# Kernel optimization log

Hardware: AMD Instinct MI355X
Metric: run time of the kernel (lower is better)

Reference implementation:

```python
import jax, jax.numpy as jnp
import numpy as np

C = 256
CQK = C // 8  # reduction_ratio = 8


def setup_inputs() -> dict:
    key = jax.random.key(0)
    ks = jax.random.split(key, 8)
    B, H, W = 8, 64, 64
    x = jax.random.normal(ks[0], (B, C, H, W), dtype=jnp.float32)
    s_in = 1.0 / np.sqrt(C)
    Wq = jax.random.normal(ks[1], (CQK, C), dtype=jnp.float32) * s_in
    bq = jax.random.normal(ks[2], (CQK,), dtype=jnp.float32) * 0.01
    Wk = jax.random.normal(ks[3], (CQK, C), dtype=jnp.float32) * s_in
    bk = jax.random.normal(ks[4], (CQK,), dtype=jnp.float32) * 0.01
    Wv = jax.random.normal(ks[5], (C, C), dtype=jnp.float32) * s_in
    bv = jax.random.normal(ks[6], (C,), dtype=jnp.float32) * 0.01
    gamma = jax.random.normal(ks[7], (1,), dtype=jnp.float32) * 0.1
    return {"x": x, "Wq": Wq, "bq": bq, "Wk": Wk, "bk": bk,
            "Wv": Wv, "bv": bv, "gamma": gamma}


def reference(x, Wq, bq, Wk, bk, Wv, bv, gamma):
    B, Cc, H, W = x.shape
    N = H * W
    xf = x.reshape(B, Cc, N)  # [B, C, N]
    # 1x1 convs == per-pixel linear maps over channels
    q = jnp.einsum('qc,bcn->bnq', Wq, xf) + bq            # [B, N, Cqk]
    k = jnp.einsum('kc,bcn->bkn', Wk, xf) + bk[None, :, None]  # [B, Cqk, N]
    v = jnp.einsum('vc,bcn->bvn', Wv, xf) + bv[None, :, None]  # [B, C, N]
    # unscaled attention scores, softmax over keys (last dim)
    scores = jax.nn.softmax(jnp.einsum('bnq,bqm->bnm', q, k), axis=-1)  # [B, N, N]
    # out[b,c,n] = sum_m v[b,c,m] * scores[b,n,m]  (torch: value @ scores^T)
    attn = jnp.einsum('bvm,bnm->bvn', v, scores)          # [B, C, N]
    out = gamma[0] * attn.reshape(B, Cc, H, W) + x
    return out
```

## Files before the change

kernel.cpp:

```cpp
#include <hip/hip_runtime.h>

static constexpr int B_   = 8;
static constexpr int C_   = 256;
static constexpr int CQK_ = 32;
static constexpr int N_   = 4096;

typedef __attribute__((ext_vector_type(4))) float f32x4;
typedef __attribute__((ext_vector_type(8))) short short8;
typedef __attribute__((ext_vector_type(2))) unsigned int u32x2;
typedef unsigned short ushort_t;

__device__ inline unsigned short f2bf(float f) {
    unsigned u = __float_as_uint(f);
    return (unsigned short)((u + 0x7FFFu + ((u >> 16) & 1u)) >> 16);
}
__device__ inline unsigned packbf(float lo, float hi) {
    return (unsigned)f2bf(lo) | ((unsigned)f2bf(hi) << 16);
}

__device__ inline int swzbits(int m) {
    return ((m & 3) << 5) | (((m >> 3) & 1) << 4);
}

template <int OFF>
__device__ inline u32x2 tr8(unsigned a) {
    u32x2 d;
    asm volatile("ds_read_b64_tr_b16 %0, %1 offset:%2"
                 : "=v"(d) : "v"(a), "i"(OFF));
    return d;
}

__device__ inline short8 mk8(u32x2 lo, u32x2 hi) {
    union { unsigned u[4]; short8 s; } v;
    v.u[0] = lo.x; v.u[1] = lo.y; v.u[2] = hi.x; v.u[3] = hi.y;
    return v.s;
}

__global__ __launch_bounds__(256) void prep_kernel(
    const float* __restrict__ Wq, const float* __restrict__ bq,
    const float* __restrict__ Wk, const float* __restrict__ bk,
    const float* __restrict__ Wv, const float* __restrict__ bv,
    ushort_t* __restrict__ Wall, float* __restrict__ ball)
{
    const int r = blockIdx.x;
    const int t = threadIdx.x;
    const float* src;
    float bsrc;
    if (r < 32)      { src = Wq + (size_t)r * C_;        bsrc = bq[r]; }
    else if (r < 64) { src = Wk + (size_t)(r - 32) * C_; bsrc = bk[r - 32]; }
    else             { src = Wv + (size_t)(r - 64) * C_; bsrc = bv[r - 64]; }
    Wall[(size_t)r * C_ + t] = f2bf(src[t]);
    if (t == 0) ball[r] = bsrc;
}

__global__ __launch_bounds__(256) void proj_kernel(
    const float* __restrict__ x,
    const ushort_t* __restrict__ Wall, const float* __restrict__ ball,
    ushort_t* __restrict__ Qb, ushort_t* __restrict__ Kb, ushort_t* __restrict__ Vb)
{
    __shared__ __align__(16) unsigned char xs[C_ * 128];
    typedef __attribute__((address_space(3))) unsigned char lds_byte;
    const unsigned sbase = (unsigned)(size_t)(lds_byte*)xs;

    const int b  = blockIdx.x & 7;
    const int n0 = (blockIdx.x >> 3) << 6;
    const int t  = threadIdx.x;

    {
        const int cst = t >> 4;
        const int n4  = (t & 15) << 2;
        const float* xb = x + (size_t)b * C_ * N_ + n0;
        #pragma unroll
        for (int i = 0; i < 16; ++i) {
            const int c = 16 * i + cst;
            float4 v = *(const float4*)(xb + (size_t)c * N_ + n4);
            u32x2 pk;
            pk.x = packbf(v.x, v.y);
            pk.y = packbf(v.z, v.w);
            *(u32x2*)(xs + c * 128 + ((n4 * 2) ^ swzbits(c))) = pk;
        }
    }
    __syncthreads();

    const int l  = t & 63, w = t >> 6;
    const int li = l & 15, g = l >> 4;
    const int rr = li >> 2, ss = l & 3;
    const int swz_tr = (rr << 5) | ((g & 1) << 4);
    const int ocb = 80 * w;

    f32x4 acc[5][4];
    #pragma unroll
    for (int i = 0; i < 5; ++i)
        #pragma unroll
        for (int j = 0; j < 4; ++j) acc[i][j] = (f32x4){0.f, 0.f, 0.f, 0.f};

    #pragma unroll 2
    for (int kg = 0; kg < 8; ++kg) {
        u32x2 pb[4][2];
        #pragma unroll
        for (int jn = 0; jn < 4; ++jn) {
            unsigned a = sbase + (32 * kg + 8 * g + rr) * 128
                       + ((32 * jn + 8 * ss) ^ swz_tr);
            pb[jn][0] = tr8<0>(a);
            pb[jn][1] = tr8<512>(a);
        }
        short8 af[5];
        #pragma unroll
        for (int tm = 0; tm < 5; ++tm)
            af[tm] = *(const short8*)(Wall + (size_t)(ocb + 16 * tm + li) * C_
                                      + 32 * kg + 8 * g);
        asm volatile("s_waitcnt lgkmcnt(0)" ::: "memory");
        __builtin_amdgcn_sched_barrier(0);
        #pragma unroll
        for (int tm = 0; tm < 5; ++tm) {
            #pragma unroll
            for (int jn = 0; jn < 4; ++jn) {
                short8 Bf = mk8(pb[jn][0], pb[jn][1]);
                acc[tm][jn] = __builtin_amdgcn_mfma_f32_16x16x32_bf16(
                                  af[tm], Bf, acc[tm][jn], 0, 0, 0);
            }
        }
    }

    #pragma unroll
    for (int tm = 0; tm < 5; ++tm) {
        const int oc0 = ocb + 16 * tm + 4 * g;
        float4 bias = *(const float4*)(ball + oc0);
        #pragma unroll
        for (int jn = 0; jn < 4; ++jn) {
            const int n = n0 + 16 * jn + li;
            f32x4 a = acc[tm][jn];
            u32x2 pk;
            pk.x = packbf(a[0] + bias.x, a[1] + bias.y);
            pk.y = packbf(a[2] + bias.z, a[3] + bias.w);
            if (oc0 < 32) {
                *(u32x2*)(Qb + (size_t)(b * N_ + n) * CQK_ + oc0) = pk;
            } else if (oc0 < 64) {
                *(u32x2*)(Kb + (size_t)(b * N_ + n) * CQK_ + (oc0 - 32)) = pk;
            } else {
                char* dst = (char*)Vb + (size_t)(b * N_ + n) * 512
                          + (((oc0 - 64) * 2) ^ swzbits(n));
                *(u32x2*)dst = pk;
            }
        }
    }
}

__global__ __launch_bounds__(256) void attn_kernel(
    const float* __restrict__ x,
    const ushort_t* __restrict__ Qb, const ushort_t* __restrict__ Kb,
    const ushort_t* __restrict__ Vb,
    const float* __restrict__ gamma, float* __restrict__ out)
{
    __shared__ __align__(16) unsigned char smem[32768 + 8192 + 256];
    unsigned char* Pl = smem + 32768;
    float* rsl = (float*)(smem + 32768 + 8192);

    typedef __attribute__((address_space(3))) unsigned char lds_byte;
    const unsigned sbase = (unsigned)(size_t)(lds_byte*)smem;

    const int b  = blockIdx.x & 7;
    const int n0 = (blockIdx.x >> 3) << 6;
    const int t  = threadIdx.x;
    const int l  = t & 63, w = t >> 6;
    const int li = l & 15, g = l >> 4;
    const int rr = li >> 2, ss = l & 3;
    const int hq = w & 1,  hc = w >> 1;
    const int swz_tr = (rr << 5) | ((g & 1) << 4);

    short8 qf = *(const short8*)(Qb + (size_t)(b * N_ + n0 + 16 * w + li) * CQK_ + 8 * g);

    f32x4 acc[2][8];
    #pragma unroll
    for (int i = 0; i < 2; ++i)
        #pragma unroll
        for (int j = 0; j < 8; ++j) acc[i][j] = (f32x4){0.f, 0.f, 0.f, 0.f};
    float rs0 = 0.f, rs1 = 0.f, rs2 = 0.f, rs3 = 0.f;

    const ushort_t* Kbb = Kb + (size_t)(b * N_) * CQK_;
    const char* Vgb = (const char*)Vb + (size_t)(b * N_) * 512;
    const f32x4 zf = {0.f, 0.f, 0.f, 0.f};

    for (int m0 = 0; m0 < N_; m0 += 64) {
        short8 kf[4];
        #pragma unroll
        for (int jm = 0; jm < 4; ++jm)
            kf[jm] = *(const short8*)(Kbb + (size_t)(m0 + 16 * jm + li) * CQK_ + 8 * g);

        {
            const char* gsrc = Vgb + (size_t)m0 * 512 + w * 1024 + l * 16;
            #pragma unroll
            for (int i = 0; i < 8; ++i)
                __builtin_amdgcn_global_load_lds(
                    (const __attribute__((address_space(1))) unsigned int*)(gsrc + i * 4096),
                    (__attribute__((address_space(3))) unsigned int*)(smem + w * 1024 + i * 4096),
                    16, 0, 0);
        }

        #pragma unroll
        for (int jm = 0; jm < 4; ++jm) {
            f32x4 s = __builtin_amdgcn_mfma_f32_16x16x32_bf16(qf, kf[jm], zf, 0, 0, 0);
            float p0 = __expf(s[0]), p1 = __expf(s[1]);
            float p2 = __expf(s[2]), p3 = __expf(s[3]);
            rs0 += p0; rs1 += p1; rs2 += p2; rs3 += p3;
            const int m = 16 * jm + li;
            u32x2 pu; pu.x = packbf(p0, p1); pu.y = packbf(p2, p3);
            *(u32x2*)(Pl + m * 128 + ((32 * w + 8 * g) ^ swzbits(m))) = pu;
        }
        __syncthreads();

        #pragma unroll
        for (int kb = 0; kb < 2; ++kb) {
            u32x2 pa[2][2], vbf[8][2];
            #pragma unroll
            for (int jq = 0; jq < 2; ++jq) {
                unsigned a = sbase + 32768u
                           + (32 * kb + 8 * g + rr) * 128
                           + ((64 * hq + 32 * jq + 8 * ss) ^ swz_tr);
                pa[jq][0] = tr8<0>(a);
                pa[jq][1] = tr8<512>(a);
            }
            #pragma unroll
            for (int jc = 0; jc < 8; ++jc) {
                unsigned a = sbase
                           + (32 * kb + 8 * g + rr) * 512
                           + ((256 * hc + 32 * jc + 8 * ss) ^ swz_tr);
                vbf[jc][0] = tr8<0>(a);
                vbf[jc][1] = tr8<2048>(a);
            }
            asm volatile("s_waitcnt lgkmcnt(0)" ::: "memory");
            __builtin_amdgcn_sched_barrier(0);
            #pragma unroll
            for (int jq = 0; jq < 2; ++jq) {
                short8 A = mk8(pa[jq][0], pa[jq][1]);
                #pragma unroll
                for (int jc = 0; jc < 8; ++jc) {
                    short8 Bf = mk8(vbf[jc][0], vbf[jc][1]);
                    acc[jq][jc] = __builtin_amdgcn_mfma_f32_16x16x32_bf16(
                                      A, Bf, acc[jq][jc], 0, 0, 0);
                }
            }
        }
        __syncthreads();
    }

    float rsv[4] = {rs0, rs1, rs2, rs3};
    #pragma unroll
    for (int r = 0; r < 4; ++r) {
        float v = rsv[r];
        v += __shfl_xor(v, 1, 64);
        v += __shfl_xor(v, 2, 64);
        v += __shfl_xor(v, 4, 64);
        v += __shfl_xor(v, 8, 64);
        rsv[r] = v;
    }
    if (li == 0) {
        rsl[16 * w + 4 * g + 0] = rsv[0];
        rsl[16 * w + 4 * g + 1] = rsv[1];
        rsl[16 * w + 4 * g + 2] = rsv[2];
        rsl[16 * w + 4 * g + 3] = rsv[3];
    }
    __syncthreads();

    float inv[2][4];
    #pragma unroll
    for (int jq = 0; jq < 2; ++jq)
        #pragma unroll
        for (int r = 0; r < 4; ++r)
            inv[jq][r] = 1.0f / rsl[32 * hq + 16 * jq + 4 * g + r];

    const float gm = gamma[0];
    #pragma unroll
    for (int jq = 0; jq < 2; ++jq)
        #pragma unroll
        for (int jc = 0; jc < 8; ++jc) {
            const int c = 128 * hc + 16 * jc + li;
            const size_t rowoff = (size_t)(b * C_ + c) * N_
                                + n0 + 32 * hq + 16 * jq + 4 * g;
            float4 xv = *(const float4*)(x + rowoff);
            f32x4 a = acc[jq][jc];
            float4 o;
            o.x = gm * a[0] * inv[jq][0] + xv.x;
            o.y = gm * a[1] * inv[jq][1] + xv.y;
            o.z = gm * a[2] * inv[jq][2] + xv.z;
            o.w = gm * a[3] * inv[jq][3] + xv.w;
            *(float4*)(out + rowoff) = o;
        }
}

extern "C" void kernel_launch(void* const* d_in, const int* in_sizes, int n_in,
                              void* d_out, int out_size, void* d_ws, size_t ws_size,
                              hipStream_t stream)
{
    const float* x     = (const float*)d_in[0];
    const float* Wq    = (const float*)d_in[1];
    const float* bq    = (const float*)d_in[2];
    const float* Wk    = (const float*)d_in[3];
    const float* bk    = (const float*)d_in[4];
    const float* Wv    = (const float*)d_in[5];
    const float* bv    = (const float*)d_in[6];
    const float* gamma = (const float*)d_in[7];
    float* out = (float*)d_out;

    ushort_t* ws = (ushort_t*)d_ws;
    ushort_t* Qb   = ws;
    ushort_t* Kb   = Qb + (size_t)B_ * N_ * CQK_;
    ushort_t* Vb   = Kb + (size_t)B_ * N_ * CQK_;
    ushort_t* Wall = Vb + (size_t)B_ * N_ * C_;
    float*    ball = (float*)(Wall + (size_t)320 * C_);

    prep_kernel<<<320, 256, 0, stream>>>(Wq, bq, Wk, bk, Wv, bv, Wall, ball);
    proj_kernel<<<B_ * (N_ / 64), 256, 0, stream>>>(x, Wall, ball, Qb, Kb, Vb);
    attn_kernel<<<B_ * (N_ / 64), 256, 0, stream>>>(x, Qb, Kb, Vb, gamma, out);
}
```

Before: 151.1 us.

## Store V channel-major and load V fragments directly from global in attention

The projection kernel now writes V transposed as [B, C, N] bf16 and computes transposed MFMA tiles for V, so the attention kernel can read V B-fragments straight from global memory into registers instead of staging them through LDS with transposing reads. Each wave now keeps its own private P tile in padded LDS, covering both query halves, which removes the block-wide __syncthreads in the key loop. Row sums are reduced with shuffles and ds_bpermute rather than a shared-memory pass. The trade-off is that each wave computes the QK scores twice (redundant exp work across the hc halves) and issues more global V loads that rely on the cache, in exchange for less LDS traffic and fewer block-wide barriers.

```diff
diff --git a/kernel.cpp b/kernel.cpp
--- a/kernel.cpp
+++ b/kernel.cpp
@@ -56,7 +56,7 @@
 __global__ __launch_bounds__(256) void proj_kernel(
     const float* __restrict__ x,
     const ushort_t* __restrict__ Wall, const float* __restrict__ ball,
-    ushort_t* __restrict__ Qb, ushort_t* __restrict__ Kb, ushort_t* __restrict__ Vb)
+    ushort_t* __restrict__ Qb, ushort_t* __restrict__ Kb, ushort_t* __restrict__ Vt)
 {
     __shared__ __align__(16) unsigned char xs[C_ * 128];
     typedef __attribute__((address_space(3))) unsigned char lds_byte;
@@ -86,7 +86,6 @@
     const int li = l & 15, g = l >> 4;
     const int rr = li >> 2, ss = l & 3;
     const int swz_tr = (rr << 5) | ((g & 1) << 4);
-    const int ocb = 80 * w;
 
     f32x4 acc[5][4];
     #pragma unroll
@@ -107,41 +106,48 @@
         short8 af[5];
         #pragma unroll
         for (int tm = 0; tm < 5; ++tm)
-            af[tm] = *(const short8*)(Wall + (size_t)(ocb + 16 * tm + li) * C_
+            af[tm] = *(const short8*)(Wall + (size_t)(16 * (4 * tm + w) + li) * C_
                                       + 32 * kg + 8 * g);
         asm volatile("s_waitcnt lgkmcnt(0)" ::: "memory");
         __builtin_amdgcn_sched_barrier(0);
         #pragma unroll
-        for (int tm = 0; tm < 5; ++tm) {
-            #pragma unroll
-            for (int jn = 0; jn < 4; ++jn) {
-                short8 Bf = mk8(pb[jn][0], pb[jn][1]);
+        for (int jn = 0; jn < 4; ++jn) {
+            short8 Bf = mk8(pb[jn][0], pb[jn][1]);
+            acc[0][jn] = __builtin_amdgcn_mfma_f32_16x16x32_bf16(
+                             af[0], Bf, acc[0][jn], 0, 0, 0);
+            #pragma unroll
+            for (int tm = 1; tm < 5; ++tm)
                 acc[tm][jn] = __builtin_amdgcn_mfma_f32_16x16x32_bf16(
-                                  af[tm], Bf, acc[tm][jn], 0, 0, 0);
-            }
-        }
-    }
-
-    #pragma unroll
-    for (int tm = 0; tm < 5; ++tm) {
-        const int oc0 = ocb + 16 * tm + 4 * g;
+                                  Bf, af[tm], acc[tm][jn], 0, 0, 0);
+        }
+    }
+
+    {
+        const int oc0 = 16 * w + 4 * g;
         float4 bias = *(const float4*)(ball + oc0);
+        ushort_t* dst = (w < 2) ? Qb : Kb;
+        const int col = (w < 2) ? oc0 : (oc0 - 32);
         #pragma unroll
         for (int jn = 0; jn < 4; ++jn) {
             const int n = n0 + 16 * jn + li;
-            f32x4 a = acc[tm][jn];
+            f32x4 a = acc[0][jn];
             u32x2 pk;
             pk.x = packbf(a[0] + bias.x, a[1] + bias.y);
             pk.y = packbf(a[2] + bias.z, a[3] + bias.w);
-            if (oc0 < 32) {
-                *(u32x2*)(Qb + (size_t)(b * N_ + n) * CQK_ + oc0) = pk;
-            } else if (oc0 < 64) {
-                *(u32x2*)(Kb + (size_t)(b * N_ + n) * CQK_ + (oc0 - 32)) = pk;
-            } else {
-                char* dst = (char*)Vb + (size_t)(b * N_ + n) * 512
-                          + (((oc0 - 64) * 2) ^ swzbits(n));
-                *(u32x2*)dst = pk;
-            }
+            *(u32x2*)(dst + (size_t)(b * N_ + n) * CQK_ + col) = pk;
+        }
+    }
+    #pragma unroll
+    for (int tm = 1; tm < 5; ++tm) {
+        const int c  = 16 * (4 * tm + w) + li - 64;
+        const float bc = ball[64 + c];
+        #pragma unroll
+        for (int jn = 0; jn < 4; ++jn) {
+            f32x4 a = acc[tm][jn];
+            u32x2 pk;
+            pk.x = packbf(a[0] + bc, a[1] + bc);
+            pk.y = packbf(a[2] + bc, a[3] + bc);
+            *(u32x2*)(Vt + (size_t)(b * C_ + c) * N_ + n0 + 16 * jn + 4 * g) = pk;
         }
     }
 }
@@ -149,36 +155,34 @@
 __global__ __launch_bounds__(256) void attn_kernel(
     const float* __restrict__ x,
     const ushort_t* __restrict__ Qb, const ushort_t* __restrict__ Kb,
-    const ushort_t* __restrict__ Vb,
+    const ushort_t* __restrict__ Vt,
     const float* __restrict__ gamma, float* __restrict__ out)
 {
-    __shared__ __align__(16) unsigned char smem[32768 + 8192 + 256];
-    unsigned char* Pl = smem + 32768;
-    float* rsl = (float*)(smem + 32768 + 8192);
-
-    typedef __attribute__((address_space(3))) unsigned char lds_byte;
-    const unsigned sbase = (unsigned)(size_t)(lds_byte*)smem;
+    __shared__ __align__(16) unsigned char Pl[4 * 32 * 144];
 
     const int b  = blockIdx.x & 7;
     const int n0 = (blockIdx.x >> 3) << 6;
     const int t  = threadIdx.x;
     const int l  = t & 63, w = t >> 6;
     const int li = l & 15, g = l >> 4;
-    const int rr = li >> 2, ss = l & 3;
     const int hq = w & 1,  hc = w >> 1;
-    const int swz_tr = (rr << 5) | ((g & 1) << 4);
-
-    short8 qf = *(const short8*)(Qb + (size_t)(b * N_ + n0 + 16 * w + li) * CQK_ + 8 * g);
+    unsigned char* Pw = Pl + w * 4608;
+    const int xorq = (li & 1) << 4;
+
+    short8 qf[2];
+    #pragma unroll
+    for (int jq = 0; jq < 2; ++jq)
+        qf[jq] = *(const short8*)(Qb + (size_t)(b * N_ + n0 + 32 * hq + 16 * jq + li) * CQK_ + 8 * g);
 
     f32x4 acc[2][8];
     #pragma unroll
     for (int i = 0; i < 2; ++i)
         #pragma unroll
         for (int j = 0; j < 8; ++j) acc[i][j] = (f32x4){0.f, 0.f, 0.f, 0.f};
-    float rs0 = 0.f, rs1 = 0.f, rs2 = 0.f, rs3 = 0.f;
+    float rs[2] = {0.f, 0.f};
 
     const ushort_t* Kbb = Kb + (size_t)(b * N_) * CQK_;
-    const char* Vgb = (const char*)Vb + (size_t)(b * N_) * 512;
+    const ushort_t* Vtb = Vt + (size_t)b * C_ * N_;
     const f32x4 zf = {0.f, 0.f, 0.f, 0.f};
 
     for (int m0 = 0; m0 < N_; m0 += 64) {
@@ -186,88 +190,76 @@
         #pragma unroll
         for (int jm = 0; jm < 4; ++jm)
             kf[jm] = *(const short8*)(Kbb + (size_t)(m0 + 16 * jm + li) * CQK_ + 8 * g);
+        short8 v0[8];
+        #pragma unroll
+        for (int jc = 0; jc < 8; ++jc)
+            v0[jc] = *(const short8*)(Vtb + (size_t)(128 * hc + 16 * jc + li) * N_
+                                      + m0 + 8 * g);
+
+        #pragma unroll
+        for (int jm = 0; jm < 4; ++jm) {
+            #pragma unroll
+            for (int jq = 0; jq < 2; ++jq) {
+                f32x4 s = __builtin_amdgcn_mfma_f32_16x16x32_bf16(kf[jm], qf[jq], zf, 0, 0, 0);
+                float p0 = __expf(s[0]), p1 = __expf(s[1]);
+                float p2 = __expf(s[2]), p3 = __expf(s[3]);
+                rs[jq] += p0 + p1 + p2 + p3;
+                u32x2 pk; pk.x = packbf(p0, p1); pk.y = packbf(p2, p3);
+                *(u32x2*)(Pw + (16 * jq + li) * 144
+                             + ((32 * jm + 8 * g) ^ xorq)) = pk;
+            }
+        }
+        asm volatile("s_waitcnt lgkmcnt(0)" ::: "memory");
+        __builtin_amdgcn_sched_barrier(0);
+
+        short8 v1[8];
+        #pragma unroll
+        for (int jc = 0; jc < 8; ++jc)
+            v1[jc] = *(const short8*)(Vtb + (size_t)(128 * hc + 16 * jc + li) * N_
+                                      + m0 + 32 + 8 * g);
 
         {
-            const char* gsrc = Vgb + (size_t)m0 * 512 + w * 1024 + l * 16;
-            #pragma unroll
-            for (int i = 0; i < 8; ++i)
-                __builtin_amdgcn_global_load_lds(
-                    (const __attribute__((address_space(1))) unsigned int*)(gsrc + i * 4096),
-                    (__attribute__((address_space(3))) unsigned int*)(smem + w * 1024 + i * 4096),
-                    16, 0, 0);
-        }
-
-        #pragma unroll
-        for (int jm = 0; jm < 4; ++jm) {
-            f32x4 s = __builtin_amdgcn_mfma_f32_16x16x32_bf16(qf, kf[jm], zf, 0, 0, 0);
-            float p0 = __expf(s[0]), p1 = __expf(s[1]);
-            float p2 = __expf(s[2]), p3 = __expf(s[3]);
-            rs0 += p0; rs1 += p1; rs2 += p2; rs3 += p3;
-            const int m = 16 * jm + li;
-            u32x2 pu; pu.x = packbf(p0, p1); pu.y = packbf(p2, p3);
-            *(u32x2*)(Pl + m * 128 + ((32 * w + 8 * g) ^ swzbits(m))) = pu;
-        }
-        __syncthreads();
-
-        #pragma unroll
-        for (int kb = 0; kb < 2; ++kb) {
-            u32x2 pa[2][2], vbf[8][2];
-            #pragma unroll
-            for (int jq = 0; jq < 2; ++jq) {
-                unsigned a = sbase + 32768u
-                           + (32 * kb + 8 * g + rr) * 128
-                           + ((64 * hq + 32 * jq + 8 * ss) ^ swz_tr);
-                pa[jq][0] = tr8<0>(a);
-                pa[jq][1] = tr8<512>(a);
-            }
-            #pragma unroll
-            for (int jc = 0; jc < 8; ++jc) {
-                unsigned a = sbase
-                           + (32 * kb + 8 * g + rr) * 512
-                           + ((256 * hc + 32 * jc + 8 * ss) ^ swz_tr);
-                vbf[jc][0] = tr8<0>(a);
-                vbf[jc][1] = tr8<2048>(a);
-            }
-            asm volatile("s_waitcnt lgkmcnt(0)" ::: "memory");
-            __builtin_amdgcn_sched_barrier(0);
-            #pragma unroll
-            for (int jq = 0; jq < 2; ++jq) {
-                short8 A = mk8(pa[jq][0], pa[jq][1]);
+            short8 pa[2];
+            #pragma unroll
+            for (int jq = 0; jq < 2; ++jq)
+                pa[jq] = *(const short8*)(Pw + (16 * jq + li) * 144
+                                             + ((16 * g) ^ xorq));
+            #pragma unroll
+            for (int jq = 0; jq < 2; ++jq)
                 #pragma unroll
-                for (int jc = 0; jc < 8; ++jc) {
-                    short8 Bf = mk8(vbf[jc][0], vbf[jc][1]);
+                for (int jc = 0; jc < 8; ++jc)
                     acc[jq][jc] = __builtin_amdgcn_mfma_f32_16x16x32_bf16(
-                                      A, Bf, acc[jq][jc], 0, 0, 0);
-                }
-            }
-        }
-        __syncthreads();
-    }
-
-    float rsv[4] = {rs0, rs1, rs2, rs3};
-    #pragma unroll
-    for (int r = 0; r < 4; ++r) {
-        float v = rsv[r];
-        v += __shfl_xor(v, 1, 64);
-        v += __shfl_xor(v, 2, 64);
-        v += __shfl_xor(v, 4, 64);
-        v += __shfl_xor(v, 8, 64);
-        rsv[r] = v;
-    }
-    if (li == 0) {
-        rsl[16 * w + 4 * g + 0] = rsv[0];
-        rsl[16 * w + 4 * g + 1] = rsv[1];
-        rsl[16 * w + 4 * g + 2] = rsv[2];
-        rsl[16 * w + 4 * g + 3] = rsv[3];
-    }
-    __syncthreads();
-
+                                      pa[jq], v0[jc], acc[jq][jc], 0, 0, 0);
+        }
+        {
+            short8 pa[2];
+            #pragma unroll
+            for (int jq = 0; jq < 2; ++jq)
+                pa[jq] = *(const short8*)(Pw + (16 * jq + li) * 144
+                                             + ((64 + 16 * g) ^ xorq));
+            #pragma unroll
+            for (int jq = 0; jq < 2; ++jq)
+                #pragma unroll
+                for (int jc = 0; jc < 8; ++jc)
+                    acc[jq][jc] = __builtin_amdgcn_mfma_f32_16x16x32_bf16(
+                                      pa[jq], v1[jc], acc[jq][jc], 0, 0, 0);
+        }
+    }
+
+    #pragma unroll
+    for (int jq = 0; jq < 2; ++jq) {
+        rs[jq] += __shfl_xor(rs[jq], 16, 64);
+        rs[jq] += __shfl_xor(rs[jq], 32, 64);
+    }
     float inv[2][4];
     #pragma unroll
     for (int jq = 0; jq < 2; ++jq)
         #pragma unroll
-        for (int r = 0; r < 4; ++r)
-            inv[jq][r] = 1.0f / rsl[32 * hq + 16 * jq + 4 * g + r];
+        for (int r = 0; r < 4; ++r) {
+            int v = __builtin_amdgcn_ds_bpermute((4 * g + r) * 4,
+                                                 __float_as_int(rs[jq]));
+            inv[jq][r] = 1.0f / __int_as_float(v);
+        }
 
     const float gm = gamma[0];
     #pragma unroll
@@ -305,11 +297,11 @@
     ushort_t* ws = (ushort_t*)d_ws;
     ushort_t* Qb   = ws;
     ushort_t* Kb   = Qb + (size_t)B_ * N_ * CQK_;
-    ushort_t* Vb   = Kb + (size_t)B_ * N_ * CQK_;
-    ushort_t* Wall = Vb + (size_t)B_ * N_ * C_;
+    ushort_t* Vt   = Kb + (size_t)B_ * N_ * CQK_;
+    ushort_t* Wall = Vt + (size_t)B_ * C_ * N_;
     float*    ball = (float*)(Wall + (size_t)320 * C_);
 
     prep_kernel<<<320, 256, 0, stream>>>(Wq, bq, Wk, bk, Wv, bv, Wall, ball);
-    proj_kernel<<<B_ * (N_ / 64), 256, 0, stream>>>(x, Wall, ball, Qb, Kb, Vb);
-    attn_kernel<<<B_ * (N_ / 64), 256, 0, stream>>>(x, Qb, Kb, Vb, gamma, out);
-}
+    proj_kernel<<<B_ * (N_ / 64), 256, 0, stream>>>(x, Wall, ball, Qb, Kb, Vt);
+    attn_kernel<<<B_ * (N_ / 64), 256, 0, stream>>>(x, Qb, Kb, Vt, gamma, out);
+}
```

Result: slower. 288.7 us (+91.1%).
